# Optimization experiments

Measured on AMD Instinct MI355X. Metric: run time of the kernel, lower is better.

Reference implementation:

```python
import jax, jax.numpy as jnp
import numpy as np

NUM_POINTS = 131072
NUM_RETAIN = 65536  # int(131072 * 0.5)


def setup_inputs() -> dict:
    key = jax.random.key(0)
    k1, k2 = jax.random.split(key)
    points = jax.random.normal(k1, (64, NUM_POINTS, 4), dtype=jnp.float32)
    dropout_weights = jax.random.normal(k2, (NUM_POINTS,), dtype=jnp.float32)
    return {"points": points, "dropout_weights": dropout_weights}


def reference(points, dropout_weights):
    # points: [B, N, C]; dropout_weights: [N]
    sampling_probs = jax.nn.softmax(dropout_weights)               # [N]
    sum_weights = jnp.sum(sampling_probs)                          # scalar (== 1 up to fp error)
    scale = sampling_probs / (sum_weights + 1e-6)                  # [N]
    downsampled = points * scale[None, :, None]                    # [B, N, C]
    # topk is identical across batch since probs are batch-independent
    _, indices = jax.lax.top_k(sampling_probs, NUM_RETAIN)         # sorted descending, like torch.topk
    return downsampled[:, indices, :]                              # [B, num_retain, C]
```

## Files before the change

kernel.cpp:

```cpp
#include <hip/hip_runtime.h>
#include <hip/hip_bf16.h>
#include <cstdint>

#define NPTS  131072
#define NRET  65536
#define NBAT  64
#define NBUCK (1 << 18)
#define BSH   14

__device__ __forceinline__ unsigned int desc_key(float w) {
    unsigned int b = __float_as_uint(w);
    unsigned int s = b ^ ((unsigned int)((int)b >> 31) | 0x80000000u);
    return ~s;
}

__global__ void k_zero_pmax(const float* __restrict__ w, uint4* __restrict__ zp,
                            float* __restrict__ pmax) {
    int j = blockIdx.x, tid = threadIdx.x;
    zp[j * 256 + tid] = make_uint4(0u, 0u, 0u, 0u);
    if (j < 256) {
        __shared__ float sm[256];
        int i = j * 256 + tid;
        float m = fmaxf(w[i], w[i + 65536]);
        sm[tid] = m; __syncthreads();
        for (int off = 128; off > 0; off >>= 1) {
            if (tid < off) sm[tid] = fmaxf(sm[tid], sm[tid + off]);
            __syncthreads();
        }
        if (tid == 0) pmax[j] = sm[0];
    }
}

__global__ void k_exp_sum(const float* __restrict__ w, const float* __restrict__ pmax,
                          float* __restrict__ e_out, float* __restrict__ bs) {
    __shared__ float smm[256];
    __shared__ float smr[256];
    int tid = threadIdx.x;
    smm[tid] = pmax[tid]; __syncthreads();
    for (int off = 128; off > 0; off >>= 1) {
        if (tid < off) smm[tid] = fmaxf(smm[tid], smm[tid + off]);
        __syncthreads();
    }
    float m = smm[0];
    int task = blockIdx.x * 256 + tid;
    int base = task >> 3;
    int k    = task & 7;
    const float* wp = w + (size_t)base * 128;
    float* ep = e_out + (size_t)base * 128;
    float r = 0.0f;
    #pragma unroll
    for (int i = 0; i < 128; i += 8) {
        float e = (float)exp((double)(wp[i + k] - m));
        ep[i + k] = e;
        r += e;
    }
    smr[tid] = r; __syncthreads();
    if (k == 0)
        bs[base] = ((smr[tid]+smr[tid+1])+(smr[tid+2]+smr[tid+3]))
                 + ((smr[tid+4]+smr[tid+5])+(smr[tid+6]+smr[tid+7]));
}

__global__ void k_prob_hist_sum(float* __restrict__ probs, const float* __restrict__ bs,
                                unsigned int* __restrict__ hist, float* __restrict__ bs2) {
    __shared__ float sf[256];
    __shared__ float smr[256];
    int tid = threadIdx.x;
    const float* b4 = bs + tid * 4;
    sf[tid] = (b4[0] + b4[1]) + (b4[2] + b4[3]);
    __syncthreads();
    for (int n = 128; n >= 1; n >>= 1) {
        float t = 0.0f;
        if (tid < n) t = sf[2*tid] + sf[2*tid+1];
        __syncthreads();
        if (tid < n) sf[tid] = t;
        __syncthreads();
    }
    const float Z = sf[0];
    __syncthreads();

    int task = blockIdx.x * 256 + tid;
    int base = task >> 3;
    int k    = task & 7;
    float* pp = probs + (size_t)base * 128;
    float r = 0.0f;
    #pragma unroll
    for (int i = 0; i < 128; i += 8) {
        float pv = pp[i + k] / Z;
        pp[i + k] = pv;
        r += pv;
        atomicAdd(&hist[desc_key(pv) >> BSH], 1u);
    }
    smr[tid] = r; __syncthreads();
    if (k == 0)
        bs2[base] = ((smr[tid]+smr[tid+1])+(smr[tid+2]+smr[tid+3]))
                  + ((smr[tid+4]+smr[tid+5])+(smr[tid+6]+smr[tid+7]));
}

__global__ void k_scan_local(const unsigned int* __restrict__ hist,
                             unsigned int* __restrict__ local,
                             unsigned int* __restrict__ chunksum) {
    __shared__ unsigned int sm[256];
    int tid = threadIdx.x;
    int g0 = (blockIdx.x * 256 + tid) * 4;
    uint4 h = *(const uint4*)&hist[g0];
    unsigned int s = h.x + h.y + h.z + h.w;
    sm[tid] = s; __syncthreads();
    for (int off = 1; off < 256; off <<= 1) {
        unsigned int t = (tid >= off) ? sm[tid - off] : 0u;
        __syncthreads();
        sm[tid] += t;
        __syncthreads();
    }
    unsigned int excl = sm[tid] - s;
    uint4 o;
    o.x = excl; o.y = excl + h.x; o.z = o.y + h.y; o.w = o.z + h.z;
    *(uint4*)&local[g0] = o;
    if (tid == 255) chunksum[blockIdx.x] = sm[255];
}

__global__ void k_scatter(const float* __restrict__ probs,
                          const unsigned int* __restrict__ local,
                          const unsigned int* __restrict__ chunksum,
                          unsigned int* __restrict__ cnt,
                          unsigned long long* __restrict__ bucketed) {
    __shared__ unsigned int su[256];
    __shared__ unsigned int sco[256];
    int tid = threadIdx.x;
    unsigned int v = chunksum[tid];
    su[tid] = v; __syncthreads();
    for (int off = 1; off < 256; off <<= 1) {
        unsigned int t = (tid >= off) ? su[tid - off] : 0u;
        __syncthreads();
        su[tid] += t;
        __syncthreads();
    }
    sco[tid] = su[tid] - v;
    __syncthreads();
    int i = blockIdx.x * 256 + tid;
    unsigned int d = desc_key(probs[i]);
    unsigned int b = d >> BSH;
    unsigned int base = sco[b >> 10] + local[b];
    unsigned int off = atomicAdd(&cnt[b], 1u);
    bucketed[base + off] = ((unsigned long long)d << 17) | (unsigned int)i;
}

__global__ void k_rank(const unsigned long long* __restrict__ bucketed,
                       const unsigned int* __restrict__ hist,
                       const unsigned int* __restrict__ local,
                       const unsigned int* __restrict__ chunksum,
                       const float* __restrict__ bs2,
                       const float* __restrict__ probs,
                       uint2* __restrict__ ret_rs) {
    __shared__ unsigned int su[256];
    __shared__ unsigned int sco[256];
    __shared__ float sf[256];
    int tid = threadIdx.x;
    unsigned int v = chunksum[tid];
    su[tid] = v;
    const float* b4 = bs2 + tid * 4;
    sf[tid] = (b4[0] + b4[1]) + (b4[2] + b4[3]);
    __syncthreads();
    for (int off = 1; off < 256; off <<= 1) {
        unsigned int t = (tid >= off) ? su[tid - off] : 0u;
        __syncthreads();
        su[tid] += t;
        __syncthreads();
    }
    sco[tid] = su[tid] - v;
    __syncthreads();
    for (int n = 128; n >= 1; n >>= 1) {
        float t = 0.0f;
        if (tid < n) t = sf[2*tid] + sf[2*tid+1];
        __syncthreads();
        if (tid < n) sf[tid] = t;
        __syncthreads();
    }
    const float inv = 1.0f / (sf[0] + 1e-6f);

    int p = blockIdx.x * 256 + tid;
    unsigned long long kk = bucketed[p];
    unsigned int b = (unsigned int)(kk >> 31);
    unsigned int start = sco[b >> 10] + local[b];
    unsigned int len = hist[b];
    unsigned int c = 0;
    for (unsigned int q = start; q < start + len; ++q)
        c += (bucketed[q] < kk) ? 1u : 0u;
    unsigned int rank = start + c;
    if (rank < NRET) {
        unsigned int idx = (unsigned int)(kk & 0x1FFFFu);
        ret_rs[rank] = make_uint2(idx, __float_as_uint(probs[idx] * inv));
    }
}

__global__ __launch_bounds__(256, 2)
void k_gather(const float4* __restrict__ pts,
              const uint2* __restrict__ ret_rs,
              float4* __restrict__ out) {
    int j = blockIdx.x;
    int v = j & 7;
    int s = j >> 3;
    int b = v + ((s >> 5) << 3);
    int r0 = ((s & 31) << 11) + threadIdx.x;
    const float4* src = pts + (size_t)b * NPTS;
    float4* dst = out + (size_t)b * NRET;

    uint2 rs0 = ret_rs[r0];
    uint2 rs1 = ret_rs[r0 + 256];
    uint2 rs2 = ret_rs[r0 + 512];
    uint2 rs3 = ret_rs[r0 + 768];
    uint2 rs4 = ret_rs[r0 + 1024];
    uint2 rs5 = ret_rs[r0 + 1280];
    uint2 rs6 = ret_rs[r0 + 1536];
    uint2 rs7 = ret_rs[r0 + 1792];
    float4 v0 = src[rs0.x]; float4 v1 = src[rs1.x];
    float4 v2 = src[rs2.x]; float4 v3 = src[rs3.x];
    float4 v4 = src[rs4.x]; float4 v5 = src[rs5.x];
    float4 v6 = src[rs6.x]; float4 v7 = src[rs7.x];
    float c0 = __uint_as_float(rs0.y); float c1 = __uint_as_float(rs1.y);
    float c2 = __uint_as_float(rs2.y); float c3 = __uint_as_float(rs3.y);
    float c4 = __uint_as_float(rs4.y); float c5 = __uint_as_float(rs5.y);
    float c6 = __uint_as_float(rs6.y); float c7 = __uint_as_float(rs7.y);
    v0.x *= c0; v0.y *= c0; v0.z *= c0; v0.w *= c0; dst[r0]        = v0;
    v1.x *= c1; v1.y *= c1; v1.z *= c1; v1.w *= c1; dst[r0 + 256]  = v1;
    v2.x *= c2; v2.y *= c2; v2.z *= c2; v2.w *= c2; dst[r0 + 512]  = v2;
    v3.x *= c3; v3.y *= c3; v3.z *= c3; v3.w *= c3; dst[r0 + 768]  = v3;
    v4.x *= c4; v4.y *= c4; v4.z *= c4; v4.w *= c4; dst[r0 + 1024] = v4;
    v5.x *= c5; v5.y *= c5; v5.z *= c5; v5.w *= c5; dst[r0 + 1280] = v5;
    v6.x *= c6; v6.y *= c6; v6.z *= c6; v6.w *= c6; dst[r0 + 1536] = v6;
    v7.x *= c7; v7.y *= c7; v7.z *= c7; v7.w *= c7; dst[r0 + 1792] = v7;
}

extern "C" void kernel_launch(void* const* d_in, const int* in_sizes, int n_in,
                              void* d_out, int out_size, void* d_ws, size_t ws_size,
                              hipStream_t stream) {
    const float* pts = (const float*)d_in[0];
    const float* w   = (const float*)d_in[1];
    float* out = (float*)d_out;

    char* ws = (char*)d_ws;
    unsigned int* hist      = (unsigned int*)(ws + 0);
    unsigned int* cnt       = (unsigned int*)(ws + (1 << 20));
    unsigned int* local     = (unsigned int*)(ws + (2 << 20));
    unsigned int* chunksum  = (unsigned int*)(ws + (3 << 20));
    float*        pmax      = (float*)(ws + (3 << 20) + 8192);
    float*        bs        = (float*)(ws + (3 << 20) + 16384);
    float*        bs2       = (float*)(ws + (3 << 20) + 24576);
    float*        probs     = (float*)(ws + (3 << 20) + (1 << 19));
    unsigned long long* bucketed = (unsigned long long*)(ws + (4 << 20));
    uint2*        ret_rs    = (uint2*)(ws + (5 << 20));

    k_zero_pmax     <<<512, 256, 0, stream>>>(w, (uint4*)ws, pmax);
    k_exp_sum       <<<32,  256, 0, stream>>>(w, pmax, probs, bs);
    k_prob_hist_sum <<<32,  256, 0, stream>>>(probs, bs, hist, bs2);
    k_scan_local    <<<256, 256, 0, stream>>>(hist, local, chunksum);
    k_scatter       <<<512, 256, 0, stream>>>(probs, local, chunksum, cnt, bucketed);
    k_rank          <<<512, 256, 0, stream>>>(bucketed, hist, local, chunksum,
                                              bs2, probs, ret_rs);
    k_gather        <<<2048, 256, 0, stream>>>((const float4*)pts, ret_rs, (float4*)out);
}
```

Measured before the change: 117.7 us.

## Fuse max reduction into exp kernel and recompute probs instead of storing

```diff
diff --git a/kernel.cpp b/kernel.cpp
--- a/kernel.cpp
+++ b/kernel.cpp
@@ -14,35 +14,28 @@
     return ~s;
 }
 
-__global__ void k_zero_pmax(const float* __restrict__ w, uint4* __restrict__ zp,
-                            float* __restrict__ pmax) {
+__global__ void k_zero_exp(const float* __restrict__ w, uint4* __restrict__ zp,
+                           float* __restrict__ e_out, float* __restrict__ bs) {
     int j = blockIdx.x, tid = threadIdx.x;
-    zp[j * 256 + tid] = make_uint4(0u, 0u, 0u, 0u);
-    if (j < 256) {
-        __shared__ float sm[256];
-        int i = j * 256 + tid;
-        float m = fmaxf(w[i], w[i + 65536]);
-        sm[tid] = m; __syncthreads();
-        for (int off = 128; off > 0; off >>= 1) {
-            if (tid < off) sm[tid] = fmaxf(sm[tid], sm[tid + off]);
-            __syncthreads();
-        }
-        if (tid == 0) pmax[j] = sm[0];
-    }
-}
-
-__global__ void k_exp_sum(const float* __restrict__ w, const float* __restrict__ pmax,
-                          float* __restrict__ e_out, float* __restrict__ bs) {
+    if (j < 512) {
+        zp[j * 256 + tid] = make_uint4(0u, 0u, 0u, 0u);
+        return;
+    }
     __shared__ float smm[256];
     __shared__ float smr[256];
-    int tid = threadIdx.x;
-    smm[tid] = pmax[tid]; __syncthreads();
+    const float4* w4 = (const float4*)w;
+    float m = -3.402823466e38f;
+    for (int i = tid; i < NPTS / 4; i += 256) {
+        float4 v = w4[i];
+        m = fmaxf(m, fmaxf(fmaxf(v.x, v.y), fmaxf(v.z, v.w)));
+    }
+    smm[tid] = m; __syncthreads();
     for (int off = 128; off > 0; off >>= 1) {
         if (tid < off) smm[tid] = fmaxf(smm[tid], smm[tid + off]);
         __syncthreads();
     }
-    float m = smm[0];
-    int task = blockIdx.x * 256 + tid;
+    m = smm[0];
+    int task = (j - 512) * 256 + tid;
     int base = task >> 3;
     int k    = task & 7;
     const float* wp = w + (size_t)base * 128;
@@ -60,7 +53,7 @@
                  + ((smr[tid+4]+smr[tid+5])+(smr[tid+6]+smr[tid+7]));
 }
 
-__global__ void k_prob_hist_sum(float* __restrict__ probs, const float* __restrict__ bs,
+__global__ void k_prob_hist_sum(const float* __restrict__ probs, const float* __restrict__ bs,
                                 unsigned int* __restrict__ hist, float* __restrict__ bs2) {
     __shared__ float sf[256];
     __shared__ float smr[256];
@@ -81,12 +74,11 @@
     int task = blockIdx.x * 256 + tid;
     int base = task >> 3;
     int k    = task & 7;
-    float* pp = probs + (size_t)base * 128;
+    const float* pp = probs + (size_t)base * 128;
     float r = 0.0f;
     #pragma unroll
     for (int i = 0; i < 128; i += 8) {
         float pv = pp[i + k] / Z;
-        pp[i + k] = pv;
         r += pv;
         atomicAdd(&hist[desc_key(pv) >> BSH], 1u);
     }
@@ -119,12 +111,14 @@
 }
 
 __global__ void k_scatter(const float* __restrict__ probs,
+                          const float* __restrict__ bs,
                           const unsigned int* __restrict__ local,
                           const unsigned int* __restrict__ chunksum,
                           unsigned int* __restrict__ cnt,
                           unsigned long long* __restrict__ bucketed) {
     __shared__ unsigned int su[256];
     __shared__ unsigned int sco[256];
+    __shared__ float sf[256];
     int tid = threadIdx.x;
     unsigned int v = chunksum[tid];
     su[tid] = v; __syncthreads();
@@ -136,8 +130,22 @@
     }
     sco[tid] = su[tid] - v;
     __syncthreads();
+    const float* b4 = bs + tid * 4;
+    sf[tid] = (b4[0] + b4[1]) + (b4[2] + b4[3]);
+    __syncthreads();
+    for (int n = 128; n >= 1; n >>= 1) {
+        float t = 0.0f;
+        if (tid < n) t = sf[2*tid] + sf[2*tid+1];
+        __syncthreads();
+        if (tid < n) sf[tid] = t;
+        __syncthreads();
+    }
+    const float Z = sf[0];
+    __syncthreads();
+
     int i = blockIdx.x * 256 + tid;
-    unsigned int d = desc_key(probs[i]);
+    float pv = probs[i] / Z;
+    unsigned int d = desc_key(pv);
     unsigned int b = d >> BSH;
     unsigned int base = sco[b >> 10] + local[b];
     unsigned int off = atomicAdd(&cnt[b], 1u);
@@ -149,7 +157,6 @@
                        const unsigned int* __restrict__ local,
                        const unsigned int* __restrict__ chunksum,
                        const float* __restrict__ bs2,
-                       const float* __restrict__ probs,
                        uint2* __restrict__ ret_rs) {
     __shared__ unsigned int su[256];
     __shared__ unsigned int sco[256];
@@ -188,7 +195,9 @@
     unsigned int rank = start + c;
     if (rank < NRET) {
         unsigned int idx = (unsigned int)(kk & 0x1FFFFu);
-        ret_rs[rank] = make_uint2(idx, __float_as_uint(probs[idx] * inv));
+        unsigned int d = (unsigned int)(kk >> 17);
+        float pv = __uint_as_float(~d ^ 0x80000000u);
+        ret_rs[rank] = make_uint2(idx, __float_as_uint(pv * inv));
     }
 }
 
@@ -242,19 +251,16 @@
     unsigned int* cnt       = (unsigned int*)(ws + (1 << 20));
     unsigned int* local     = (unsigned int*)(ws + (2 << 20));
     unsigned int* chunksum  = (unsigned int*)(ws + (3 << 20));
-    float*        pmax      = (float*)(ws + (3 << 20) + 8192);
     float*        bs        = (float*)(ws + (3 << 20) + 16384);
     float*        bs2       = (float*)(ws + (3 << 20) + 24576);
     float*        probs     = (float*)(ws + (3 << 20) + (1 << 19));
     unsigned long long* bucketed = (unsigned long long*)(ws + (4 << 20));
     uint2*        ret_rs    = (uint2*)(ws + (5 << 20));
 
-    k_zero_pmax     <<<512, 256, 0, stream>>>(w, (uint4*)ws, pmax);
-    k_exp_sum       <<<32,  256, 0, stream>>>(w, pmax, probs, bs);
+    k_zero_exp      <<<544, 256, 0, stream>>>(w, (uint4*)ws, probs, bs);
     k_prob_hist_sum <<<32,  256, 0, stream>>>(probs, bs, hist, bs2);
     k_scan_local    <<<256, 256, 0, stream>>>(hist, local, chunksum);
-    k_scatter       <<<512, 256, 0, stream>>>(probs, local, chunksum, cnt, bucketed);
-    k_rank          <<<512, 256, 0, stream>>>(bucketed, hist, local, chunksum,
-                                              bs2, probs, ret_rs);
+    k_scatter       <<<512, 256, 0, stream>>>(probs, bs, local, chunksum, cnt, bucketed);
+    k_rank          <<<512, 256, 0, stream>>>(bucketed, hist, local, chunksum, bs2, ret_rs);
     k_gather        <<<2048, 256, 0, stream>>>((const float4*)pts, ret_rs, (float4*)out);
 }
```

After: 132.9 us. 1.13x slower.
